# Kernel tuning notes

Hardware: AMD Instinct MI355X
Metric: run time of the kernel (lower is better)

The kernel has to match this reference:

```python
import jax, jax.numpy as jnp
import numpy as np

D_PARAM = 20   # module's d
S1 = 1         # module's s1
D_WIN = D_PARAM + S1   # 21: sliding-window size -> 441 displacement channels
PAD = D_PARAM // 2     # 10


def setup_inputs() -> dict:
    key = jax.random.key(0)
    k1, k2 = jax.random.split(key)
    B, C, W, H = 4, 128, 128, 128
    x1 = jax.random.normal(k1, (B, C, W, H), dtype=jnp.float32)
    x2 = jax.random.normal(k2, (B, C, W, H), dtype=jnp.float32)
    return {"x1": x1, "x2": x2}


def _correlation(x1, x2):
    # out[b, di*D+dj, i, j] = sum_c x1_padded[b, c, i+di, j+dj] * x2[b, c, i, j]
    # This reproduces: pad x1 by PAD, unfold 21x21 windows stride 1, and for each
    # pixel take the dot product over channels with x2[b,:,i,j] (the 1x1 conv2d
    # in the original triple loop). Flatten order of torch is (di, dj) row-major.
    b, c, w, h = x1.shape
    x1p = jnp.pad(x1, ((0, 0), (0, 0), (PAD, PAD), (PAD, PAD)))  # [b,c,w+20,h+20]
    rows_out = []
    for di in range(D_WIN):  # small fixed displacement loop (21 iters)
        rows = jax.lax.slice_in_dim(x1p, di, di + w, axis=2)  # [b,c,w,h+20]
        # stack 21 horizontal shifts -> [b,c,w,h,D_WIN]
        win = jnp.stack(
            [jax.lax.slice_in_dim(rows, dj, dj + h, axis=3) for dj in range(D_WIN)],
            axis=-1,
        )
        # contract over channels: [b, D_WIN(dj), w, h]
        rows_out.append(jnp.einsum('bcwhd,bcwh->bdwh', win, x2))
    out = jnp.stack(rows_out, axis=1)  # [b, D_WIN(di), D_WIN(dj), w, h]
    return out.reshape(b, D_WIN * D_WIN, w, h)


def reference(x1, x2):
    return _correlation(x1, x2)
```

## Files before the change

### kernel.cpp

```cpp
#include <hip/hip_runtime.h>


#define NB 4
#define NC 128
#define NW 128
#define NH 128
#define DW 21
#define PAD 10
#define NROW_T 148
#define NCOL_T 160
#define NCH 441
#define PS 37
#define SCOLS 52
#define SUS (SCOLS * NC)
#define ROW_US (NCOL_T * NC)

typedef __attribute__((ext_vector_type(8))) short short8;
typedef __attribute__((ext_vector_type(4))) float float4v;

__device__ inline ushort f2bf(float f) {
    union { float f; uint u; } v; v.f = f;
    const uint u = v.u;
    return (ushort)((u + 0x7fffu + ((u >> 16) & 1u)) >> 16);
}

__device__ inline void async_copy16(const void* g, void* l) {
    __builtin_amdgcn_global_load_lds(
        (const __attribute__((address_space(1))) void*)g,
        (__attribute__((address_space(3))) void*)l, 16, 0, 0);
}

__device__ inline void stage_row(const ushort* src, ushort* dst, int t) {
    const char* s = (const char*)src;
    char* d = (char*)dst;
    #pragma unroll
    for (int it = 0; it < 3; ++it) {
        const int off = it * 4096 + t * 16;
        async_copy16(s + off, d + off);
    }
    if (t < 64) {
        const int off = 12288 + t * 16;
        async_copy16(s + off, d + off);
    }
}

__global__ __launch_bounds__(256) void transpose_x1(const float* __restrict__ x1,
                                                    ushort* __restrict__ x1T) {
    __shared__ uint tile[128][65];
    const int t = threadIdx.x;
    const int b = blockIdx.x / NROW_T;
    const int r = blockIdx.x % NROW_T;
    const int w = r - PAD;
    const bool inr = (w >= 0 && w < NW);
    if (inr) {
        #pragma unroll
        for (int it = 0; it < 8; ++it) {
            const int u = it * 256 + t;
            const int g4 = u & 31;
            const int cp = u >> 5;
            const float4 va = *(const float4*)&x1[(((size_t)b * NC + 2 * cp    ) * NW + w) * NH + g4 * 4];
            const float4 vb = *(const float4*)&x1[(((size_t)b * NC + 2 * cp + 1) * NW + w) * NH + g4 * 4];
            tile[g4 * 4 + 0][cp] = (uint)f2bf(va.x) | ((uint)f2bf(vb.x) << 16);
            tile[g4 * 4 + 1][cp] = (uint)f2bf(va.y) | ((uint)f2bf(vb.y) << 16);
            tile[g4 * 4 + 2][cp] = (uint)f2bf(va.z) | ((uint)f2bf(vb.z) << 16);
            tile[g4 * 4 + 3][cp] = (uint)f2bf(va.w) | ((uint)f2bf(vb.w) << 16);
        }
    }
    __syncthreads();
    #pragma unroll
    for (int it = 0; it < 10; ++it) {
        const int u = it * 256 + t;
        const int cg = u & 15;
        const int col = u >> 4;
        uint4 v = make_uint4(0, 0, 0, 0);
        const int h = col - PAD;
        if (inr && h >= 0 && h < NH) {
            v.x = tile[h][cg * 4 + 0];
            v.y = tile[h][cg * 4 + 1];
            v.z = tile[h][cg * 4 + 2];
            v.w = tile[h][cg * 4 + 3];
        }
        const int chunk = cg ^ (col & 15);
        *(uint4*)&x1T[(((size_t)b * NROW_T + r) * NCOL_T + col) * NC + chunk * 8] = v;
    }
}

__global__ __launch_bounds__(256) void corr_mfma(const ushort* __restrict__ x1T,
                                                 const float* __restrict__ x2,
                                                 float* __restrict__ out) {
    __shared__ ushort win[5][SUS];
    __shared__ float patch[4][16 * PS];

    const int t = threadIdx.x;
    const int wave = t >> 6;
    const int lane = t & 63;
    const int n16 = lane & 15;
    const int q = lane >> 4;

    const int n = blockIdx.x;
    const int b = (n & 7) >> 1;
    const int ihalf = n & 1;
    const int slot = n >> 3;
    const int iq = ihalf * 16 + (slot >> 2);
    const int jq = slot & 3;
    const int i0 = iq * 4;
    const int col0 = jq * 32;
    const int i = i0 + wave;

    const ushort* xbase = x1T + (size_t)(b * NROW_T) * ROW_US + (size_t)col0 * NC;

    #pragma unroll
    for (int r = 0; r < 4; ++r)
        stage_row(xbase + (size_t)(i0 + r) * ROW_US, win[r], t);

    short8 Bf[2][4];
    #pragma unroll
    for (int nt = 0; nt < 2; ++nt) {
        const int jc = col0 + nt * 16 + n16;
        #pragma unroll
        for (int k4 = 0; k4 < 4; ++k4) {
            short8 s;
            #pragma unroll
            for (int e = 0; e < 8; ++e) {
                const int c = k4 * 32 + q * 8 + e;
                s[e] = (short)f2bf(x2[(((size_t)b * NC + c) * NW + i) * NH + jc]);
            }
            Bf[nt][k4] = s;
        }
    }

    __syncthreads();

    float* P = &patch[wave][0];

    for (int di = 0; di < DW; ++di) {
        const ushort* A = win[(di + wave) % 5];

        short8 Af[4][4];
        #pragma unroll
        for (int k4 = 0; k4 < 4; ++k4) {
            const int kc = q + 4 * k4;
            #pragma unroll
            for (int tl = 0; tl < 4; ++tl) {
                const int base = (tl < 3) ? tl * 16 : 36;
                const int c = base + n16;
                Af[tl][k4] = *(const short8*)&A[c * NC + ((kc ^ (c & 15)) & 15) * 8];
            }
        }

        if (di < DW - 1)
            stage_row(xbase + (size_t)(i0 + di + 4) * ROW_US, win[(di + 4) % 5], t);

        float4v a00 = {0.f,0.f,0.f,0.f}, a01 = {0.f,0.f,0.f,0.f}, a02 = {0.f,0.f,0.f,0.f};
        float4v a10 = {0.f,0.f,0.f,0.f}, a11 = {0.f,0.f,0.f,0.f}, a12 = {0.f,0.f,0.f,0.f};
        #pragma unroll
        for (int k4 = 0; k4 < 4; ++k4) {
            a00 = __builtin_amdgcn_mfma_f32_16x16x32_bf16(Af[0][k4], Bf[0][k4], a00, 0, 0, 0);
            a01 = __builtin_amdgcn_mfma_f32_16x16x32_bf16(Af[1][k4], Bf[0][k4], a01, 0, 0, 0);
            a02 = __builtin_amdgcn_mfma_f32_16x16x32_bf16(Af[2][k4], Bf[0][k4], a02, 0, 0, 0);
            a10 = __builtin_amdgcn_mfma_f32_16x16x32_bf16(Af[1][k4], Bf[1][k4], a10, 0, 0, 0);
            a11 = __builtin_amdgcn_mfma_f32_16x16x32_bf16(Af[2][k4], Bf[1][k4], a11, 0, 0, 0);
            a12 = __builtin_amdgcn_mfma_f32_16x16x32_bf16(Af[3][k4], Bf[1][k4], a12, 0, 0, 0);
        }

        #pragma unroll
        for (int nt = 0; nt < 2; ++nt) {
            const float4v va = nt ? a10 : a00;
            const float4v vb = nt ? a11 : a01;
            const float4v vc = nt ? a12 : a02;
            #pragma unroll
            for (int reg = 0; reg < 4; ++reg) {
                P[n16 * PS + q * 4 + reg]      = va[reg];
                P[n16 * PS + 16 + q * 4 + reg] = vb[reg];
            }
            if (q == (nt ? 3 : 0)) {
                #pragma unroll
                for (int reg = 0; reg < 4; ++reg)
                    P[n16 * PS + 32 + reg] = vc[reg];
            }
            #pragma unroll
            for (int it2 = 0; it2 < 2; ++it2) {
                const int u = it2 * 64 + lane;
                if (u < 84) {
                    const int dj = u >> 2;
                    const int jj = (u & 3) * 4;
                    float4v v;
                    #pragma unroll
                    for (int p = 0; p < 4; ++p)
                        v[p] = P[(jj + p) * (PS + 1) + dj];
                    *(float4v*)&out[(((size_t)(b * NCH + di * DW + dj)) * NW + i) * NH
                                    + col0 + nt * 16 + jj] = v;
                }
            }
        }

        __syncthreads();
    }
}

extern "C" void kernel_launch(void* const* d_in, const int* in_sizes, int n_in,
                              void* d_out, int out_size, void* d_ws, size_t ws_size,
                              hipStream_t stream) {
    const float* x1 = (const float*)d_in[0];
    const float* x2 = (const float*)d_in[1];
    float* out = (float*)d_out;
    ushort* x1T = (ushort*)d_ws;
    transpose_x1<<<dim3(NB * NROW_T), dim3(256), 0, stream>>>(x1, x1T);
    corr_mfma<<<dim3(NB * 32 * 4), dim3(256), 0, stream>>>(x1T, x2, out);
}
```

Measured before the change: 184.9 us.

## Reuse each staged x1 row's fragments across four output rows via staggered wave schedule

Each wave now keeps x2 B-fragments for all four output rows of the block in registers. A-fragments loaded from one staged x1 row are reused across those four rows in a skewed 27-step pipeline, so LDS fragment reads drop roughly fourfold. The LDS ring shrinks from 5 to 3 row buffers, and the MFMA/epilogue work moves into a helper that uses vectorized float4 patch stores (PS changed to 36). The cost is more loop steps with barriers, pipeline fill and drain idle steps, and much higher VGPR pressure under launch_bounds(256,2).

```diff
diff --git a/kernel.cpp b/kernel.cpp
--- a/kernel.cpp
+++ b/kernel.cpp
@@ -10,10 +10,11 @@
 #define NROW_T 148
 #define NCOL_T 160
 #define NCH 441
-#define PS 37
+#define PS 36
 #define SCOLS 52
 #define SUS (SCOLS * NC)
 #define ROW_US (NCOL_T * NC)
+#define NBUF 3
 
 typedef __attribute__((ext_vector_type(8))) short short8;
 typedef __attribute__((ext_vector_type(4))) float float4v;
@@ -85,10 +86,52 @@
     }
 }
 
-__global__ __launch_bounds__(256) void corr_mfma(const ushort* __restrict__ x1T,
-                                                 const float* __restrict__ x2,
-                                                 float* __restrict__ out) {
-    __shared__ ushort win[5][SUS];
+__device__ __forceinline__ void do_pair(const short8 (&Af)[4][4],
+                                        const short8 (&Bfp)[2][4],
+                                        float* P, float* __restrict__ out,
+                                        int b, int di, int i, int col0,
+                                        int n16, int q, int lane) {
+    float4v a00 = {0.f,0.f,0.f,0.f}, a01 = {0.f,0.f,0.f,0.f}, a02 = {0.f,0.f,0.f,0.f};
+    float4v a10 = {0.f,0.f,0.f,0.f}, a11 = {0.f,0.f,0.f,0.f}, a12 = {0.f,0.f,0.f,0.f};
+    #pragma unroll
+    for (int k4 = 0; k4 < 4; ++k4) {
+        a00 = __builtin_amdgcn_mfma_f32_16x16x32_bf16(Af[0][k4], Bfp[0][k4], a00, 0, 0, 0);
+        a01 = __builtin_amdgcn_mfma_f32_16x16x32_bf16(Af[1][k4], Bfp[0][k4], a01, 0, 0, 0);
+        a02 = __builtin_amdgcn_mfma_f32_16x16x32_bf16(Af[2][k4], Bfp[0][k4], a02, 0, 0, 0);
+        a10 = __builtin_amdgcn_mfma_f32_16x16x32_bf16(Af[1][k4], Bfp[1][k4], a10, 0, 0, 0);
+        a11 = __builtin_amdgcn_mfma_f32_16x16x32_bf16(Af[2][k4], Bfp[1][k4], a11, 0, 0, 0);
+        a12 = __builtin_amdgcn_mfma_f32_16x16x32_bf16(Af[3][k4], Bfp[1][k4], a12, 0, 0, 0);
+    }
+    #pragma unroll
+    for (int nt = 0; nt < 2; ++nt) {
+        const float4v va = nt ? a10 : a00;
+        const float4v vb = nt ? a11 : a01;
+        const float4v vc = nt ? a12 : a02;
+        *(float4v*)&P[n16 * PS + q * 4]      = va;
+        *(float4v*)&P[n16 * PS + 16 + q * 4] = vb;
+        if (q == (nt ? 3 : 0))
+            *(float4v*)&P[n16 * PS + 32] = vc;
+        #pragma unroll
+        for (int it2 = 0; it2 < 2; ++it2) {
+            const int u = it2 * 64 + lane;
+            if (u < 84) {
+                const int dj = u >> 2;
+                const int jj = (u & 3) * 4;
+                float4v v;
+                #pragma unroll
+                for (int pp = 0; pp < 4; ++pp)
+                    v[pp] = P[(jj + pp) * (PS + 1) + dj];
+                *(float4v*)&out[(((size_t)(b * NCH + di * DW + dj)) * NW + i) * NH
+                                + col0 + nt * 16 + jj] = v;
+            }
+        }
+    }
+}
+
+__global__ __launch_bounds__(256, 2) void corr_mfma(const ushort* __restrict__ x1T,
+                                                    const float* __restrict__ x2,
+                                                    float* __restrict__ out) {
+    __shared__ ushort win[NBUF][SUS];
     __shared__ float patch[4][16 * PS];
 
     const int t = threadIdx.x;
@@ -105,95 +148,70 @@
     const int jq = slot & 3;
     const int i0 = iq * 4;
     const int col0 = jq * 32;
-    const int i = i0 + wave;
 
     const ushort* xbase = x1T + (size_t)(b * NROW_T) * ROW_US + (size_t)col0 * NC;
 
-    #pragma unroll
-    for (int r = 0; r < 4; ++r)
-        stage_row(xbase + (size_t)(i0 + r) * ROW_US, win[r], t);
-
-    short8 Bf[2][4];
-    #pragma unroll
-    for (int nt = 0; nt < 2; ++nt) {
-        const int jc = col0 + nt * 16 + n16;
-        #pragma unroll
-        for (int k4 = 0; k4 < 4; ++k4) {
-            short8 s;
-            #pragma unroll
-            for (int e = 0; e < 8; ++e) {
-                const int c = k4 * 32 + q * 8 + e;
-                s[e] = (short)f2bf(x2[(((size_t)b * NC + c) * NW + i) * NH + jc]);
-            }
-            Bf[nt][k4] = s;
-        }
-    }
-
-    __syncthreads();
-
-    float* P = &patch[wave][0];
-
-    for (int di = 0; di < DW; ++di) {
-        const ushort* A = win[(di + wave) % 5];
-
-        short8 Af[4][4];
-        #pragma unroll
-        for (int k4 = 0; k4 < 4; ++k4) {
-            const int kc = q + 4 * k4;
-            #pragma unroll
-            for (int tl = 0; tl < 4; ++tl) {
-                const int base = (tl < 3) ? tl * 16 : 36;
-                const int c = base + n16;
-                Af[tl][k4] = *(const short8*)&A[c * NC + ((kc ^ (c & 15)) & 15) * 8];
-            }
-        }
-
-        if (di < DW - 1)
-            stage_row(xbase + (size_t)(i0 + di + 4) * ROW_US, win[(di + 4) % 5], t);
-
-        float4v a00 = {0.f,0.f,0.f,0.f}, a01 = {0.f,0.f,0.f,0.f}, a02 = {0.f,0.f,0.f,0.f};
-        float4v a10 = {0.f,0.f,0.f,0.f}, a11 = {0.f,0.f,0.f,0.f}, a12 = {0.f,0.f,0.f,0.f};
-        #pragma unroll
-        for (int k4 = 0; k4 < 4; ++k4) {
-            a00 = __builtin_amdgcn_mfma_f32_16x16x32_bf16(Af[0][k4], Bf[0][k4], a00, 0, 0, 0);
-            a01 = __builtin_amdgcn_mfma_f32_16x16x32_bf16(Af[1][k4], Bf[0][k4], a01, 0, 0, 0);
-            a02 = __builtin_amdgcn_mfma_f32_16x16x32_bf16(Af[2][k4], Bf[0][k4], a02, 0, 0, 0);
-            a10 = __builtin_amdgcn_mfma_f32_16x16x32_bf16(Af[1][k4], Bf[1][k4], a10, 0, 0, 0);
-            a11 = __builtin_amdgcn_mfma_f32_16x16x32_bf16(Af[2][k4], Bf[1][k4], a11, 0, 0, 0);
-            a12 = __builtin_amdgcn_mfma_f32_16x16x32_bf16(Af[3][k4], Bf[1][k4], a12, 0, 0, 0);
-        }
-
+    stage_row(xbase + (size_t)i0 * ROW_US, win[0], t);
+    stage_row(xbase + (size_t)(i0 + 1) * ROW_US, win[1], t);
+
+    short8 Bf[4][2][4];
+    #pragma unroll
+    for (int ii = 0; ii < 4; ++ii) {
         #pragma unroll
         for (int nt = 0; nt < 2; ++nt) {
-            const float4v va = nt ? a10 : a00;
-            const float4v vb = nt ? a11 : a01;
-            const float4v vc = nt ? a12 : a02;
+            const int jc = col0 + nt * 16 + n16;
             #pragma unroll
-            for (int reg = 0; reg < 4; ++reg) {
-                P[n16 * PS + q * 4 + reg]      = va[reg];
-                P[n16 * PS + 16 + q * 4 + reg] = vb[reg];
+            for (int k4 = 0; k4 < 4; ++k4) {
+                short8 sv;
+                #pragma unroll
+                for (int e = 0; e < 8; ++e) {
+                    const int c = k4 * 32 + q * 8 + e;
+                    sv[e] = (short)f2bf(x2[(((size_t)b * NC + c) * NW + (i0 + ii)) * NH + jc]);
+                }
+                Bf[ii][nt][k4] = sv;
             }
-            if (q == (nt ? 3 : 0)) {
+        }
+    }
+
+    __syncthreads();
+
+    short8 Af[4][4];
+    float* P = &patch[wave][0];
+
+    for (int s = 0; s < 27; ++s) {
+        if (s + 2 <= 23)
+            stage_row(xbase + (size_t)(i0 + s + 2) * ROW_US, win[(s + 2) % NBUF], t);
+
+        const int d = s - wave;
+        const int p = d & 3;
+        const int r = s - p;
+
+        if (d >= 0 && r <= 23) {
+            if (p == 0) {
+                const ushort* A = win[r % NBUF];
                 #pragma unroll
-                for (int reg = 0; reg < 4; ++reg)
-                    P[n16 * PS + 32 + reg] = vc[reg];
+                for (int k4 = 0; k4 < 4; ++k4) {
+                    const int kc = q + 4 * k4;
+                    #pragma unroll
+                    for (int tl = 0; tl < 4; ++tl) {
+                        const int base = (tl < 3) ? tl * 16 : 36;
+                        const int c = base + n16;
+                        Af[tl][k4] = *(const short8*)&A[c * NC + ((kc ^ (c & 15)) & 15) * 8];
+                    }
+                }
+                if (r <= 20)
+                    do_pair(Af, Bf[0], P, out, b, r,     i0,     col0, n16, q, lane);
+            } else if (p == 1) {
+                if (r >= 1 && r <= 21)
+                    do_pair(Af, Bf[1], P, out, b, r - 1, i0 + 1, col0, n16, q, lane);
+            } else if (p == 2) {
+                if (r >= 2 && r <= 22)
+                    do_pair(Af, Bf[2], P, out, b, r - 2, i0 + 2, col0, n16, q, lane);
+            } else {
+                if (r >= 3)
+                    do_pair(Af, Bf[3], P, out, b, r - 3, i0 + 3, col0, n16, q, lane);
             }
-            #pragma unroll
-            for (int it2 = 0; it2 < 2; ++it2) {
-                const int u = it2 * 64 + lane;
-                if (u < 84) {
-                    const int dj = u >> 2;
-                    const int jj = (u & 3) * 4;
-                    float4v v;
-                    #pragma unroll
-                    for (int p = 0; p < 4; ++p)
-                        v[p] = P[(jj + p) * (PS + 1) + dj];
-                    *(float4v*)&out[(((size_t)(b * NCH + di * DW + dj)) * NW + i) * NH
-                                    + col0 + nt * 16 + jj] = v;
-                }
-            }
-        }
-
+        }
         __syncthreads();
     }
 }
```

Result: slower. 203.5 us (+10.0%).

## Read x1 windows directly from global memory and split displacement rows across blocks

Applied to the files above, without the earlier changes.

Drops the LDS ring buffer with async global-to-LDS row staging and its per-iteration block barrier. Each wave now loads its A fragments straight from the bf16 transposed x1 in global or L2, and the XOR swizzle is removed from the transpose. The grid doubles so each block covers half of the 21 di rows, which raises parallelism and sets occupancy to 3 blocks per CU. The cost is redundant global/L2 traffic for overlapping rows and reloading x2 fragments twice per tile.

```diff
diff --git a/kernel.cpp b/kernel.cpp
--- a/kernel.cpp
+++ b/kernel.cpp
@@ -11,8 +11,6 @@
 #define NCOL_T 160
 #define NCH 441
 #define PS 37
-#define SCOLS 52
-#define SUS (SCOLS * NC)
 #define ROW_US (NCOL_T * NC)
 
 typedef __attribute__((ext_vector_type(8))) short short8;
@@ -22,26 +20,6 @@
     union { float f; uint u; } v; v.f = f;
     const uint u = v.u;
     return (ushort)((u + 0x7fffu + ((u >> 16) & 1u)) >> 16);
-}
-
-__device__ inline void async_copy16(const void* g, void* l) {
-    __builtin_amdgcn_global_load_lds(
-        (const __attribute__((address_space(1))) void*)g,
-        (__attribute__((address_space(3))) void*)l, 16, 0, 0);
-}
-
-__device__ inline void stage_row(const ushort* src, ushort* dst, int t) {
-    const char* s = (const char*)src;
-    char* d = (char*)dst;
-    #pragma unroll
-    for (int it = 0; it < 3; ++it) {
-        const int off = it * 4096 + t * 16;
-        async_copy16(s + off, d + off);
-    }
-    if (t < 64) {
-        const int off = 12288 + t * 16;
-        async_copy16(s + off, d + off);
-    }
 }
 
 __global__ __launch_bounds__(256) void transpose_x1(const float* __restrict__ x1,
@@ -80,15 +58,13 @@
             v.z = tile[h][cg * 4 + 2];
             v.w = tile[h][cg * 4 + 3];
         }
-        const int chunk = cg ^ (col & 15);
-        *(uint4*)&x1T[(((size_t)b * NROW_T + r) * NCOL_T + col) * NC + chunk * 8] = v;
+        *(uint4*)&x1T[(((size_t)b * NROW_T + r) * NCOL_T + col) * NC + cg * 8] = v;
     }
 }
 
-__global__ __launch_bounds__(256) void corr_mfma(const ushort* __restrict__ x1T,
-                                                 const float* __restrict__ x2,
-                                                 float* __restrict__ out) {
-    __shared__ ushort win[5][SUS];
+__global__ __launch_bounds__(256, 3) void corr_mfma(const ushort* __restrict__ x1T,
+                                                    const float* __restrict__ x2,
+                                                    float* __restrict__ out) {
     __shared__ float patch[4][16 * PS];
 
     const int t = threadIdx.x;
@@ -101,17 +77,14 @@
     const int b = (n & 7) >> 1;
     const int ihalf = n & 1;
     const int slot = n >> 3;
-    const int iq = ihalf * 16 + (slot >> 2);
-    const int jq = slot & 3;
+    const int dihalf = slot & 1;
+    const int jq = (slot >> 1) & 3;
+    const int iq = ihalf * 16 + (slot >> 3);
     const int i0 = iq * 4;
     const int col0 = jq * 32;
     const int i = i0 + wave;
-
-    const ushort* xbase = x1T + (size_t)(b * NROW_T) * ROW_US + (size_t)col0 * NC;
-
-    #pragma unroll
-    for (int r = 0; r < 4; ++r)
-        stage_row(xbase + (size_t)(i0 + r) * ROW_US, win[r], t);
+    const int di0 = dihalf ? 11 : 0;
+    const int diN = dihalf ? 21 : 11;
 
     short8 Bf[2][4];
     #pragma unroll
@@ -129,38 +102,37 @@
         }
     }
 
-    __syncthreads();
+    float* P = &patch[wave][0];
+    const ushort* Abase = x1T + ((size_t)(b * NROW_T) * NCOL_T + col0) * NC;
 
-    float* P = &patch[wave][0];
+    for (int di = di0; di < diN; ++di) {
+        const ushort* A = Abase + (size_t)(i0 + wave + di) * ROW_US;
 
-    for (int di = 0; di < DW; ++di) {
-        const ushort* A = win[(di + wave) % 5];
+        float4v a00 = {0.f,0.f,0.f,0.f}, a01 = {0.f,0.f,0.f,0.f}, a02 = {0.f,0.f,0.f,0.f};
+        float4v a10 = {0.f,0.f,0.f,0.f}, a11 = {0.f,0.f,0.f,0.f}, a12 = {0.f,0.f,0.f,0.f};
 
-        short8 Af[4][4];
         #pragma unroll
-        for (int k4 = 0; k4 < 4; ++k4) {
-            const int kc = q + 4 * k4;
+        for (int kh = 0; kh < 2; ++kh) {
+            short8 Ah[4][2];
             #pragma unroll
             for (int tl = 0; tl < 4; ++tl) {
                 const int base = (tl < 3) ? tl * 16 : 36;
-                const int c = base + n16;
-                Af[tl][k4] = *(const short8*)&A[c * NC + ((kc ^ (c & 15)) & 15) * 8];
+                #pragma unroll
+                for (int j = 0; j < 2; ++j) {
+                    const int k4 = kh * 2 + j;
+                    Ah[tl][j] = *(const short8*)&A[(base + n16) * NC + (q + 4 * k4) * 8];
+                }
             }
-        }
-
-        if (di < DW - 1)
-            stage_row(xbase + (size_t)(i0 + di + 4) * ROW_US, win[(di + 4) % 5], t);
-
-        float4v a00 = {0.f,0.f,0.f,0.f}, a01 = {0.f,0.f,0.f,0.f}, a02 = {0.f,0.f,0.f,0.f};
-        float4v a10 = {0.f,0.f,0.f,0.f}, a11 = {0.f,0.f,0.f,0.f}, a12 = {0.f,0.f,0.f,0.f};
-        #pragma unroll
-        for (int k4 = 0; k4 < 4; ++k4) {
-            a00 = __builtin_amdgcn_mfma_f32_16x16x32_bf16(Af[0][k4], Bf[0][k4], a00, 0, 0, 0);
-            a01 = __builtin_amdgcn_mfma_f32_16x16x32_bf16(Af[1][k4], Bf[0][k4], a01, 0, 0, 0);
-            a02 = __builtin_amdgcn_mfma_f32_16x16x32_bf16(Af[2][k4], Bf[0][k4], a02, 0, 0, 0);
-            a10 = __builtin_amdgcn_mfma_f32_16x16x32_bf16(Af[1][k4], Bf[1][k4], a10, 0, 0, 0);
-            a11 = __builtin_amdgcn_mfma_f32_16x16x32_bf16(Af[2][k4], Bf[1][k4], a11, 0, 0, 0);
-            a12 = __builtin_amdgcn_mfma_f32_16x16x32_bf16(Af[3][k4], Bf[1][k4], a12, 0, 0, 0);
+            #pragma unroll
+            for (int j = 0; j < 2; ++j) {
+                const int k4 = kh * 2 + j;
+                a00 = __builtin_amdgcn_mfma_f32_16x16x32_bf16(Ah[0][j], Bf[0][k4], a00, 0, 0, 0);
+                a01 = __builtin_amdgcn_mfma_f32_16x16x32_bf16(Ah[1][j], Bf[0][k4], a01, 0, 0, 0);
+                a02 = __builtin_amdgcn_mfma_f32_16x16x32_bf16(Ah[2][j], Bf[0][k4], a02, 0, 0, 0);
+                a10 = __builtin_amdgcn_mfma_f32_16x16x32_bf16(Ah[1][j], Bf[1][k4], a10, 0, 0, 0);
+                a11 = __builtin_amdgcn_mfma_f32_16x16x32_bf16(Ah[2][j], Bf[1][k4], a11, 0, 0, 0);
+                a12 = __builtin_amdgcn_mfma_f32_16x16x32_bf16(Ah[3][j], Bf[1][k4], a12, 0, 0, 0);
+            }
         }
 
         #pragma unroll
@@ -193,8 +165,6 @@
                 }
             }
         }
-
-        __syncthreads();
     }
 }
 
@@ -206,5 +176,5 @@
     float* out = (float*)d_out;
     ushort* x1T = (ushort*)d_ws;
     transpose_x1<<<dim3(NB * NROW_T), dim3(256), 0, stream>>>(x1, x1T);
-    corr_mfma<<<dim3(NB * 32 * 4), dim3(256), 0, stream>>>(x1T, x2, out);
+    corr_mfma<<<dim3(NB * 32 * 4 * 2), dim3(256), 0, stream>>>(x1T, x2, out);
 }
```

New measurement: 242.1 us. 1.31x slower.

## Split displacement rows across two blocks and shrink LDS ring to raise occupancy

Applied to the files above, without the earlier changes.

The 21 vertical displacements are split into two halves handled by separate blocks, doubling the grid from 512 to 1024 blocks. Each wave processes displacement `s - wave`, so a single staged x1 row in LDS is shared by all four waves. This cuts the LDS ring from 5 to 3 buffers, and `__launch_bounds__(256, 3)` asks for three resident blocks per CU. The aim is more parallelism and better latency hiding for the output-store-heavy loop. The cost is that both halves reload the x2 fragments and some x1 rows, and waves sit idle during the ramp-in and ramp-out steps of the staggered schedule.

```diff
diff --git a/kernel.cpp b/kernel.cpp
--- a/kernel.cpp
+++ b/kernel.cpp
@@ -14,6 +14,7 @@
 #define SCOLS 52
 #define SUS (SCOLS * NC)
 #define ROW_US (NCOL_T * NC)
+#define NBUF 3
 
 typedef __attribute__((ext_vector_type(8))) short short8;
 typedef __attribute__((ext_vector_type(4))) float float4v;
@@ -85,10 +86,10 @@
     }
 }
 
-__global__ __launch_bounds__(256) void corr_mfma(const ushort* __restrict__ x1T,
-                                                 const float* __restrict__ x2,
-                                                 float* __restrict__ out) {
-    __shared__ ushort win[5][SUS];
+__global__ __launch_bounds__(256, 3) void corr_mfma(const ushort* __restrict__ x1T,
+                                                    const float* __restrict__ x2,
+                                                    float* __restrict__ out) {
+    __shared__ ushort win[NBUF][SUS];
     __shared__ float patch[4][16 * PS];
 
     const int t = threadIdx.x;
@@ -101,17 +102,22 @@
     const int b = (n & 7) >> 1;
     const int ihalf = n & 1;
     const int slot = n >> 3;
-    const int iq = ihalf * 16 + (slot >> 2);
-    const int jq = slot & 3;
+    const int dihalf = slot & 1;
+    const int jq = (slot >> 1) & 3;
+    const int iq = ihalf * 16 + (slot >> 3);
     const int i0 = iq * 4;
     const int col0 = jq * 32;
     const int i = i0 + wave;
 
-    const ushort* xbase = x1T + (size_t)(b * NROW_T) * ROW_US + (size_t)col0 * NC;
-
-    #pragma unroll
-    for (int r = 0; r < 4; ++r)
-        stage_row(xbase + (size_t)(i0 + r) * ROW_US, win[r], t);
+    const int s0    = dihalf ? 11 : 0;
+    const int s_end = dihalf ? 23 : 13;
+    const int dlo   = dihalf ? 11 : 0;
+    const int dhi   = dihalf ? 20 : 10;
+
+    const ushort* xbase = x1T + (size_t)(b * NROW_T + i0) * ROW_US + (size_t)col0 * NC;
+
+    stage_row(xbase + (size_t)s0 * ROW_US, win[s0 % NBUF], t);
+    stage_row(xbase + (size_t)(s0 + 1) * ROW_US, win[(s0 + 1) % NBUF], t);
 
     short8 Bf[2][4];
     #pragma unroll
@@ -133,63 +139,69 @@
 
     float* P = &patch[wave][0];
 
-    for (int di = 0; di < DW; ++di) {
-        const ushort* A = win[(di + wave) % 5];
+    for (int s = s0; s <= s_end; ++s) {
+        const int di = s - wave;
+        const bool act = (di >= dlo) && (di <= dhi);
 
         short8 Af[4][4];
-        #pragma unroll
-        for (int k4 = 0; k4 < 4; ++k4) {
-            const int kc = q + 4 * k4;
-            #pragma unroll
-            for (int tl = 0; tl < 4; ++tl) {
-                const int base = (tl < 3) ? tl * 16 : 36;
-                const int c = base + n16;
-                Af[tl][k4] = *(const short8*)&A[c * NC + ((kc ^ (c & 15)) & 15) * 8];
-            }
-        }
-
-        if (di < DW - 1)
-            stage_row(xbase + (size_t)(i0 + di + 4) * ROW_US, win[(di + 4) % 5], t);
-
-        float4v a00 = {0.f,0.f,0.f,0.f}, a01 = {0.f,0.f,0.f,0.f}, a02 = {0.f,0.f,0.f,0.f};
-        float4v a10 = {0.f,0.f,0.f,0.f}, a11 = {0.f,0.f,0.f,0.f}, a12 = {0.f,0.f,0.f,0.f};
-        #pragma unroll
-        for (int k4 = 0; k4 < 4; ++k4) {
-            a00 = __builtin_amdgcn_mfma_f32_16x16x32_bf16(Af[0][k4], Bf[0][k4], a00, 0, 0, 0);
-            a01 = __builtin_amdgcn_mfma_f32_16x16x32_bf16(Af[1][k4], Bf[0][k4], a01, 0, 0, 0);
-            a02 = __builtin_amdgcn_mfma_f32_16x16x32_bf16(Af[2][k4], Bf[0][k4], a02, 0, 0, 0);
-            a10 = __builtin_amdgcn_mfma_f32_16x16x32_bf16(Af[1][k4], Bf[1][k4], a10, 0, 0, 0);
-            a11 = __builtin_amdgcn_mfma_f32_16x16x32_bf16(Af[2][k4], Bf[1][k4], a11, 0, 0, 0);
-            a12 = __builtin_amdgcn_mfma_f32_16x16x32_bf16(Af[3][k4], Bf[1][k4], a12, 0, 0, 0);
-        }
-
-        #pragma unroll
-        for (int nt = 0; nt < 2; ++nt) {
-            const float4v va = nt ? a10 : a00;
-            const float4v vb = nt ? a11 : a01;
-            const float4v vc = nt ? a12 : a02;
-            #pragma unroll
-            for (int reg = 0; reg < 4; ++reg) {
-                P[n16 * PS + q * 4 + reg]      = va[reg];
-                P[n16 * PS + 16 + q * 4 + reg] = vb[reg];
-            }
-            if (q == (nt ? 3 : 0)) {
+        if (act) {
+            const ushort* A = win[s % NBUF];
+            #pragma unroll
+            for (int k4 = 0; k4 < 4; ++k4) {
+                const int kc = q + 4 * k4;
                 #pragma unroll
-                for (int reg = 0; reg < 4; ++reg)
-                    P[n16 * PS + 32 + reg] = vc[reg];
-            }
-            #pragma unroll
-            for (int it2 = 0; it2 < 2; ++it2) {
-                const int u = it2 * 64 + lane;
-                if (u < 84) {
-                    const int dj = u >> 2;
-                    const int jj = (u & 3) * 4;
-                    float4v v;
+                for (int tl = 0; tl < 4; ++tl) {
+                    const int base = (tl < 3) ? tl * 16 : 36;
+                    const int c = base + n16;
+                    Af[tl][k4] = *(const short8*)&A[c * NC + ((kc ^ (c & 15)) & 15) * 8];
+                }
+            }
+        }
+
+        if (s + 2 <= s_end)
+            stage_row(xbase + (size_t)(s + 2) * ROW_US, win[(s + 2) % NBUF], t);
+
+        if (act) {
+            float4v a00 = {0.f,0.f,0.f,0.f}, a01 = {0.f,0.f,0.f,0.f}, a02 = {0.f,0.f,0.f,0.f};
+            float4v a10 = {0.f,0.f,0.f,0.f}, a11 = {0.f,0.f,0.f,0.f}, a12 = {0.f,0.f,0.f,0.f};
+            #pragma unroll
+            for (int k4 = 0; k4 < 4; ++k4) {
+                a00 = __builtin_amdgcn_mfma_f32_16x16x32_bf16(Af[0][k4], Bf[0][k4], a00, 0, 0, 0);
+                a01 = __builtin_amdgcn_mfma_f32_16x16x32_bf16(Af[1][k4], Bf[0][k4], a01, 0, 0, 0);
+                a02 = __builtin_amdgcn_mfma_f32_16x16x32_bf16(Af[2][k4], Bf[0][k4], a02, 0, 0, 0);
+                a10 = __builtin_amdgcn_mfma_f32_16x16x32_bf16(Af[1][k4], Bf[1][k4], a10, 0, 0, 0);
+                a11 = __builtin_amdgcn_mfma_f32_16x16x32_bf16(Af[2][k4], Bf[1][k4], a11, 0, 0, 0);
+                a12 = __builtin_amdgcn_mfma_f32_16x16x32_bf16(Af[3][k4], Bf[1][k4], a12, 0, 0, 0);
+            }
+
+            #pragma unroll
+            for (int nt = 0; nt < 2; ++nt) {
+                const float4v va = nt ? a10 : a00;
+                const float4v vb = nt ? a11 : a01;
+                const float4v vc = nt ? a12 : a02;
+                #pragma unroll
+                for (int reg = 0; reg < 4; ++reg) {
+                    P[n16 * PS + q * 4 + reg]      = va[reg];
+                    P[n16 * PS + 16 + q * 4 + reg] = vb[reg];
+                }
+                if (q == (nt ? 3 : 0)) {
                     #pragma unroll
-                    for (int p = 0; p < 4; ++p)
-                        v[p] = P[(jj + p) * (PS + 1) + dj];
-                    *(float4v*)&out[(((size_t)(b * NCH + di * DW + dj)) * NW + i) * NH
-                                    + col0 + nt * 16 + jj] = v;
+                    for (int reg = 0; reg < 4; ++reg)
+                        P[n16 * PS + 32 + reg] = vc[reg];
+                }
+                #pragma unroll
+                for (int it2 = 0; it2 < 2; ++it2) {
+                    const int u = it2 * 64 + lane;
+                    if (u < 84) {
+                        const int dj = u >> 2;
+                        const int jj = (u & 3) * 4;
+                        float4v v;
+                        #pragma unroll
+                        for (int p = 0; p < 4; ++p)
+                            v[p] = P[(jj + p) * (PS + 1) + dj];
+                        *(float4v*)&out[(((size_t)(b * NCH + di * DW + dj)) * NW + i) * NH
+                                        + col0 + nt * 16 + jj] = v;
+                    }
                 }
             }
         }
@@ -206,5 +218,5 @@
     float* out = (float*)d_out;
     ushort* x1T = (ushort*)d_ws;
     transpose_x1<<<dim3(NB * NROW_T), dim3(256), 0, stream>>>(x1, x1T);
-    corr_mfma<<<dim3(NB * 32 * 4), dim3(256), 0, stream>>>(x1T, x2, out);
-}
+    corr_mfma<<<dim3(NB * 32 * 4 * 2), dim3(256), 0, stream>>>(x1T, x2, out);
+}
```

After: 193.4 us. 4.6% more time.
